# Kernel optimization log

Measured on AMD Instinct MI355X. Metric: run time of the kernel, lower is better.

## Reference

```python
import jax, jax.numpy as jnp
import numpy as np

N_NODES = 100000
N_EDGES = 1600000
D_IN = 128
D_HID = 128
N_CLASS = 10
N_GRAPHS = 512
BN_EPS = 1e-5


def setup_inputs() -> dict:
    key = jax.random.key(0)
    ks = jax.random.split(key, 12)
    x = jax.random.normal(ks[0], (N_NODES, D_IN), dtype=jnp.float32)
    edge_index = jax.random.randint(ks[1], (2, N_EDGES), 0, N_NODES, dtype=jnp.int32)
    idx = jnp.sort(jax.random.randint(ks[2], (N_NODES,), 0, N_GRAPHS, dtype=jnp.int32))
    s = 1.0 / np.sqrt(D_HID)
    W1 = jax.random.uniform(ks[3], (D_IN, D_HID), minval=-s, maxval=s, dtype=jnp.float32)
    b1 = jnp.zeros((D_HID,), jnp.float32)
    W2 = jax.random.uniform(ks[4], (D_HID, D_HID), minval=-s, maxval=s, dtype=jnp.float32)
    b2 = jnp.zeros((D_HID,), jnp.float32)
    W3 = jax.random.uniform(ks[5], (D_HID, D_HID), minval=-s, maxval=s, dtype=jnp.float32)
    b3 = jnp.zeros((D_HID,), jnp.float32)
    W4 = jax.random.uniform(ks[6], (D_HID, N_CLASS), minval=-s, maxval=s, dtype=jnp.float32)
    b4 = jnp.zeros((N_CLASS,), jnp.float32)
    gamma = jnp.ones((D_HID,), jnp.float32)
    beta = jnp.zeros((D_HID,), jnp.float32)
    return {"x": x, "edge_index": edge_index, "idx": idx,
            "W1": W1, "b1": b1, "W2": W2, "b2": b2,
            "W3": W3, "b3": b3, "W4": W4, "b4": b4,
            "gamma": gamma, "beta": beta}


def _agg(h, src, dst):
    # (adj + I) @ h : sum of neighbor features plus self-loop
    return jax.ops.segment_sum(h[src], dst, num_segments=N_NODES) + h


def reference(x, edge_index, idx, W1, b1, W2, b2, W3, b3, W4, b4, gamma, beta):
    src, dst = edge_index[0], edge_index[1]
    z1 = jax.nn.relu(_agg(x, src, dst) @ W1 + b1)          # [N, H] (dropout = identity, eval)
    h = _agg(z1, src, dst) @ W2 + b2                        # [N, H]
    pooled = jax.ops.segment_sum(h, idx, num_segments=N_GRAPHS)  # [G, H] scatter-add readout
    # BatchNorm1d over graph (batch) dimension, training-mode batch stats
    mean = jnp.mean(pooled, axis=0)
    var = jnp.var(pooled, axis=0)
    out = (pooled - mean) * jax.lax.rsqrt(var + BN_EPS) * gamma + beta
    zg = jax.nn.relu(out @ W3 + b3)
    logits = zg @ W4 + b4                                   # [G, C]
    return jax.nn.log_softmax(logits, axis=1)
```

## Files before the change

kernel.cpp:

```cpp
#include <hip/hip_runtime.h>
#include <hip/hip_fp16.h>
#include <math.h>

#define NN 100000
#define NE 1600000
#define DH 128
#define NG 512
#define NC 10
#define NSEG 8
#define SEGN 12500
#define CHE 8192
#define NCH 196
#define MAXDEG 48
#define WPITCH 136

#define NB_HIST (NCH * NSEG)
#define NB_CNT  98
#define NB_GEMM ((NN + 63) / 64)

typedef __attribute__((ext_vector_type(8))) _Float16 f16x8;
typedef __attribute__((ext_vector_type(4))) float f32x4;


__global__ __launch_bounds__(256, 3) void k_build(
    const int* __restrict__ dst, const int* __restrict__ src,
    int* __restrict__ counts, int* __restrict__ csr,
    const int* __restrict__ gidx, int* __restrict__ cnt,
    const float* __restrict__ A, const float* __restrict__ W,
    __half* __restrict__ out) {
    int b = blockIdx.x;
    int t = threadIdx.x;
    if (b < NB_HIST) {
        int seg = b & 7;
        int chunk = b >> 3;
        int lo = seg * SEGN, hi = lo + SEGN;
        int e0 = chunk * CHE;
        int e1 = e0 + CHE < NE ? e0 + CHE : NE;
        for (int e = e0 + t * 4; e < e1; e += 1024) {
            int4 d4 = *(const int4*)(dst + e);
            bool i0 = d4.x >= lo && d4.x < hi;
            bool i1 = d4.y >= lo && d4.y < hi;
            bool i2 = d4.z >= lo && d4.z < hi;
            bool i3 = d4.w >= lo && d4.w < hi;
            int4 s4 = {0, 0, 0, 0};
            if (i0 | i1 | i2 | i3) s4 = *(const int4*)(src + e);
            if (i0) {
                int p = atomicAdd(&counts[d4.x], 1);
                if (p < MAXDEG) csr[d4.x * MAXDEG + p] = s4.x;
            }
            if (i1) {
                int p = atomicAdd(&counts[d4.y], 1);
                if (p < MAXDEG) csr[d4.y * MAXDEG + p] = s4.y;
            }
            if (i2) {
                int p = atomicAdd(&counts[d4.z], 1);
                if (p < MAXDEG) csr[d4.z * MAXDEG + p] = s4.z;
            }
            if (i3) {
                int p = atomicAdd(&counts[d4.w], 1);
                if (p < MAXDEG) csr[d4.w * MAXDEG + p] = s4.w;
            }
        }
    } else if (b < NB_HIST + NB_CNT) {
        int cb = b - NB_HIST;
        int n0 = cb * 1024 + t * 4;
        if (n0 >= NN) return;
        int g = gidx[n0];
        int run = 1;
        for (int j = 1; j < 4; ++j) {
            int n = n0 + j;
            if (n < NN) {
                int gg = gidx[n];
                if (gg == g) {
                    run++;
                } else {
                    atomicAdd(&cnt[g], run);
                    g = gg;
                    run = 1;
                }
            }
        }
        atomicAdd(&cnt[g], run);
    } else {
        __shared__ _Float16 sWT[DH * WPITCH];
        __shared__ __align__(16) _Float16 sOut[4][16][DH];
        int gb = b - (NB_HIST + NB_CNT);
        int wv = t >> 6;
        int lane = t & 63;
        for (int i = t; i < DH * DH; i += 256) {
            int k = i >> 7, n = i & 127;
            sWT[n * WPITCH + k] = (_Float16)W[i];
        }
        __syncthreads();

        int m = lane & 15;
        int quad = lane >> 4;
        int node0 = gb * 64 + wv * 16;
        int nodeA = node0 + m;
        if (nodeA >= NN) nodeA = NN - 1;
        const float* arow = A + (size_t)nodeA * DH;

        f16x8 afrag[4];
#pragma unroll
        for (int kt = 0; kt < 4; ++kt) {
            int k0 = kt * 32 + quad * 8;
            float4 u0 = *(const float4*)(arow + k0);
            float4 u1 = *(const float4*)(arow + k0 + 4);
            afrag[kt][0] = (_Float16)u0.x; afrag[kt][1] = (_Float16)u0.y;
            afrag[kt][2] = (_Float16)u0.z; afrag[kt][3] = (_Float16)u0.w;
            afrag[kt][4] = (_Float16)u1.x; afrag[kt][5] = (_Float16)u1.y;
            afrag[kt][6] = (_Float16)u1.z; afrag[kt][7] = (_Float16)u1.w;
        }

#pragma unroll
        for (int ct = 0; ct < 8; ++ct) {
            f32x4 acc = {0.f, 0.f, 0.f, 0.f};
            int n = ct * 16 + m;
#pragma unroll
            for (int kt = 0; kt < 4; ++kt) {
                int k0 = kt * 32 + quad * 8;
                f16x8 bfrag = *(const f16x8*)&sWT[n * WPITCH + k0];
                acc = __builtin_amdgcn_mfma_f32_16x16x32_f16(afrag[kt], bfrag, acc, 0, 0, 0);
            }
#pragma unroll
            for (int r = 0; r < 4; ++r)
                sOut[wv][quad * 4 + r][ct * 16 + m] = (_Float16)acc[r];
        }
        __syncthreads();

        const uint4* so = (const uint4*)&sOut[wv][0][0];
        for (int i = lane; i < 256; i += 64) {
            int row = i >> 4;
            int node = node0 + row;
            if (node < NN) ((uint4*)out)[(size_t)node * 16 + (i & 15)] = so[i];
        }
    }
}


__device__ __forceinline__ void acc8(float* a, const uint4& v, float m) {
    float2 f;
    f = __half22float2(*(const __half2*)&v.x); a[0] = fmaf(m, f.x, a[0]); a[1] = fmaf(m, f.y, a[1]);
    f = __half22float2(*(const __half2*)&v.y); a[2] = fmaf(m, f.x, a[2]); a[3] = fmaf(m, f.y, a[3]);
    f = __half22float2(*(const __half2*)&v.z); a[4] = fmaf(m, f.x, a[4]); a[5] = fmaf(m, f.y, a[5]);
    f = __half22float2(*(const __half2*)&v.w); a[6] = fmaf(m, f.x, a[6]); a[7] = fmaf(m, f.y, a[7]);
}


__global__ __launch_bounds__(256, 4) void k_agg_h(
    const __half* __restrict__ in, const int* __restrict__ counts,
    const int* __restrict__ csr, const float* __restrict__ bias,
    __half* __restrict__ outA) {
    int t = threadIdx.x;
    int lane = t & 15;
    int node = blockIdx.x * 16 + (t >> 4);
    const uint4* in4 = (const uint4*)in;
    float a[8];
#pragma unroll
    for (int j = 0; j < 8; ++j) a[j] = 0.f;
    uint4 sv = in4[(size_t)node * 16 + lane];
    acc8(a, sv, 1.f);
    int e0 = node * MAXDEG;
    int deg = counts[node];
    deg = deg < MAXDEG ? deg : MAXDEG;
    int e1 = e0 + deg;
    int elast = e1 - 1;
    for (int e = e0; e < e1; e += 8) {
        int idx[8];
        float m[8];
#pragma unroll
        for (int i = 0; i < 8; ++i) {
            int ei = e + i;
            int ec = ei < elast ? ei : elast;
            idx[i] = csr[ec];
            m[i] = (ei < e1) ? 1.f : 0.f;
        }
        uint4 v[8];
#pragma unroll
        for (int i = 0; i < 8; ++i) v[i] = in4[(size_t)idx[i] * 16 + lane];
#pragma unroll
        for (int i = 0; i < 8; ++i) acc8(a, v[i], m[i]);
    }
    float4 b0 = ((const float4*)bias)[lane * 2];
    float4 b1v = ((const float4*)bias)[lane * 2 + 1];
    a[0] = fmaxf(a[0] + b0.x, 0.f);  a[1] = fmaxf(a[1] + b0.y, 0.f);
    a[2] = fmaxf(a[2] + b0.z, 0.f);  a[3] = fmaxf(a[3] + b0.w, 0.f);
    a[4] = fmaxf(a[4] + b1v.x, 0.f); a[5] = fmaxf(a[5] + b1v.y, 0.f);
    a[6] = fmaxf(a[6] + b1v.z, 0.f); a[7] = fmaxf(a[7] + b1v.w, 0.f);
    uint4 o;
    *(__half2*)&o.x = __floats2half2_rn(a[0], a[1]);
    *(__half2*)&o.y = __floats2half2_rn(a[2], a[3]);
    *(__half2*)&o.z = __floats2half2_rn(a[4], a[5]);
    *(__half2*)&o.w = __floats2half2_rn(a[6], a[7]);
    ((uint4*)outA)[(size_t)node * 16 + lane] = o;
}


__global__ __launch_bounds__(256, 4) void k_agg_pool_h(
    const __half* __restrict__ in, const int* __restrict__ counts,
    const int* __restrict__ csr, const int* __restrict__ gidx,
    float* __restrict__ pp8) {
    __shared__ __align__(16) float sA[16][DH];
    int t = threadIdx.x;
    int lane = t & 15;
    int p = t >> 4;
    int node0 = blockIdx.x * 16;
    int node = node0 + p;
    const uint4* in4 = (const uint4*)in;
    float a[8];
#pragma unroll
    for (int j = 0; j < 8; ++j) a[j] = 0.f;
    uint4 sv = in4[(size_t)node * 16 + lane];
    acc8(a, sv, 1.f);
    int e0 = node * MAXDEG;
    int deg = counts[node];
    deg = deg < MAXDEG ? deg : MAXDEG;
    int e1 = e0 + deg;
    int elast = e1 - 1;
    for (int e = e0; e < e1; e += 8) {
        int idx[8];
        float m[8];
#pragma unroll
        for (int i = 0; i < 8; ++i) {
            int ei = e + i;
            int ec = ei < elast ? ei : elast;
            idx[i] = csr[ec];
            m[i] = (ei < e1) ? 1.f : 0.f;
        }
        uint4 v[8];
#pragma unroll
        for (int i = 0; i < 8; ++i) v[i] = in4[(size_t)idx[i] * 16 + lane];
#pragma unroll
        for (int i = 0; i < 8; ++i) acc8(a, v[i], m[i]);
    }
    float4* row = (float4*)&sA[p][lane * 8];
    row[0] = make_float4(a[0], a[1], a[2], a[3]);
    row[1] = make_float4(a[4], a[5], a[6], a[7]);
    __syncthreads();
    if (t < DH) {
        float* pp = pp8 + (size_t)(blockIdx.x & 7) * NG * DH;
        int gprev = gidx[node0];
        float run = 0.f;
        for (int q = 0; q < 16; ++q) {
            int g = gidx[node0 + q];
            if (g != gprev) {
                atomicAdd(&pp[gprev * DH + t], run);
                run = 0.f;
                gprev = g;
            }
            run += sA[q][t];
        }
        atomicAdd(&pp[gprev * DH + t], run);
    }
}


__device__ __forceinline__ void fma4(float4& acc, float s, const float4& wv) {
    acc.x = fmaf(s, wv.x, acc.x);
    acc.y = fmaf(s, wv.y, acc.y);
    acc.z = fmaf(s, wv.z, acc.z);
    acc.w = fmaf(s, wv.w, acc.w);
}


__global__ __launch_bounds__(256, 2) void k_pool_mm(
    const float* __restrict__ pp8, const float* __restrict__ W,
    const float* __restrict__ bias, const int* __restrict__ cnt,
    float* __restrict__ pooled) {
    __shared__ __align__(16) float sW[DH * DH];
    __shared__ __align__(16) float sA[32 * DH];
    int t = threadIdx.x;
    int g0 = blockIdx.x * 32;
    {
        const float4* W4g = (const float4*)W;
        float4* sW4 = (float4*)sW;
        for (int i = t; i < DH * DH / 4; i += 256) sW4[i] = W4g[i];
        const float4* P4 = (const float4*)pp8;
        float4* sA4 = (float4*)sA;
        for (int i = t; i < 32 * DH / 4; i += 256) {
            float4 s;
            s.x = 0.f; s.y = 0.f; s.z = 0.f; s.w = 0.f;
#pragma unroll
            for (int c = 0; c < NSEG; ++c) {
                float4 v = P4[(size_t)c * NG * DH / 4 + (size_t)g0 * DH / 4 + i];
                s.x += v.x; s.y += v.y; s.z += v.z; s.w += v.w;
            }
            sA4[i] = s;
        }
    }
    __syncthreads();

    int c4 = t & 31;
    int n0 = (t >> 5) * 4;
    const float4* sA4 = (const float4*)sA;
    const float4* sW4 = (const float4*)sW;
    float4 acc0, acc1, acc2, acc3;
    acc0.x = acc0.y = acc0.z = acc0.w = 0.f;
    acc1 = acc0; acc2 = acc0; acc3 = acc0;

#pragma unroll 2
    for (int kc = 0; kc < DH / 4; ++kc) {
        float4 a0 = sA4[(n0 + 0) * 32 + kc];
        float4 a1 = sA4[(n0 + 1) * 32 + kc];
        float4 a2 = sA4[(n0 + 2) * 32 + kc];
        float4 a3 = sA4[(n0 + 3) * 32 + kc];
        float4 w0 = sW4[(4 * kc + 0) * 32 + c4];
        float4 w1 = sW4[(4 * kc + 1) * 32 + c4];
        float4 w2 = sW4[(4 * kc + 2) * 32 + c4];
        float4 w3 = sW4[(4 * kc + 3) * 32 + c4];
        fma4(acc0, a0.x, w0); fma4(acc0, a0.y, w1); fma4(acc0, a0.z, w2); fma4(acc0, a0.w, w3);
        fma4(acc1, a1.x, w0); fma4(acc1, a1.y, w1); fma4(acc1, a1.z, w2); fma4(acc1, a1.w, w3);
        fma4(acc2, a2.x, w0); fma4(acc2, a2.y, w1); fma4(acc2, a2.z, w2); fma4(acc2, a2.w, w3);
        fma4(acc3, a3.x, w0); fma4(acc3, a3.y, w1); fma4(acc3, a3.z, w2); fma4(acc3, a3.w, w3);
    }

    float4 b2v = ((const float4*)bias)[c4];
    float c0 = (float)cnt[g0 + n0 + 0];
    float c1 = (float)cnt[g0 + n0 + 1];
    float c2 = (float)cnt[g0 + n0 + 2];
    float c3 = (float)cnt[g0 + n0 + 3];
    fma4(acc0, c0, b2v);
    fma4(acc1, c1, b2v);
    fma4(acc2, c2, b2v);
    fma4(acc3, c3, b2v);

    float4* out4 = (float4*)pooled;
    out4[(size_t)(g0 + n0 + 0) * 32 + c4] = acc0;
    out4[(size_t)(g0 + n0 + 1) * 32 + c4] = acc1;
    out4[(size_t)(g0 + n0 + 2) * 32 + c4] = acc2;
    out4[(size_t)(g0 + n0 + 3) * 32 + c4] = acc3;
}


__global__ void k_bnstats(const float* __restrict__ pooled, float* __restrict__ mean,
                          float* __restrict__ rstd) {
    int c = blockIdx.x;
    int l = threadIdx.x;
    float s = 0.f, s2 = 0.f;
    for (int g = l; g < NG; g += 64) {
        float v = pooled[g * DH + c];
        s += v;
        s2 += v * v;
    }
#pragma unroll
    for (int off = 32; off > 0; off >>= 1) {
        s += __shfl_down(s, off, 64);
        s2 += __shfl_down(s2, off, 64);
    }
    if (l == 0) {
        float m = s * (1.f / NG);
        float var = s2 * (1.f / NG) - m * m;
        mean[c] = m;
        rstd[c] = rsqrtf(var + 1e-5f);
    }
}


__global__ __launch_bounds__(128) void k_tail(
    const float* __restrict__ pooled, const float* __restrict__ mean,
    const float* __restrict__ rstd, const float* __restrict__ gamma,
    const float* __restrict__ beta, const float* __restrict__ W3,
    const float* __restrict__ b3, const float* __restrict__ W4,
    const float* __restrict__ b4, float* __restrict__ out) {
    __shared__ __align__(16) float sW[DH * DH];
    __shared__ float sg[DH];
    __shared__ float sz[DH];
    __shared__ float slog[NC];
    __shared__ float slse;
    int g = blockIdx.x, t = threadIdx.x;
    {
        const float4* W34 = (const float4*)W3;
        float4* sW4 = (float4*)sW;
        for (int i = t; i < DH * DH / 4; i += 128) sW4[i] = W34[i];
    }
    float v = pooled[g * DH + t];
    v = (v - mean[t]) * rstd[t] * gamma[t] + beta[t];
    sg[t] = v;
    __syncthreads();
    float acc = b3[t];
#pragma unroll 4
    for (int k = 0; k < DH; ++k) acc = fmaf(sg[k], sW[k * DH + t], acc);
    sz[t] = fmaxf(acc, 0.f);
    __syncthreads();
    if (t < NC) {
        float a = b4[t];
        for (int k = 0; k < DH; ++k) a = fmaf(sz[k], W4[k * NC + t], a);
        slog[t] = a;
    }
    __syncthreads();
    if (t == 0) {
        float mx = slog[0];
        for (int j = 1; j < NC; ++j) mx = fmaxf(mx, slog[j]);
        float se = 0.f;
        for (int j = 0; j < NC; ++j) se += expf(slog[j] - mx);
        slse = mx + logf(se);
    }
    __syncthreads();
    if (t < NC) out[g * NC + t] = slog[t] - slse;
}


extern "C" void kernel_launch(void* const* d_in, const int* in_sizes, int n_in,
                              void* d_out, int out_size, void* d_ws, size_t ws_size,
                              hipStream_t stream) {
    const float* x = (const float*)d_in[0];
    const int* ei = (const int*)d_in[1];
    const int* src = ei;
    const int* dst = ei + NE;
    const int* gidx = (const int*)d_in[2];
    const float* W1 = (const float*)d_in[3];
    const float* b1 = (const float*)d_in[4];
    const float* W2 = (const float*)d_in[5];
    const float* b2 = (const float*)d_in[6];
    const float* W3 = (const float*)d_in[7];
    const float* b3 = (const float*)d_in[8];
    const float* W4 = (const float*)d_in[9];
    const float* b4 = (const float*)d_in[10];
    const float* gamma = (const float*)d_in[11];
    const float* beta = (const float*)d_in[12];
    float* out = (float*)d_out;

    char* w = (char*)d_ws;
    auto take = [&](size_t bytes) {
        char* p = w;
        w += (bytes + 255) & ~size_t(255);
        return p;
    };
    int* counts = (int*)take((size_t)NN * 4);
    int* cnt = (int*)take((size_t)NG * 4);
    float* pp8 = (float*)take((size_t)NSEG * NG * DH * 4);
    size_t zero_bytes = (size_t)((char*)(pp8 + (size_t)NSEG * NG * DH) - (char*)counts);
    int* csr = (int*)take((size_t)NN * MAXDEG * 4);
    __half* y = (__half*)take((size_t)NN * DH * 2);
    __half* z1 = (__half*)take((size_t)NN * DH * 2);
    float* pooled = (float*)take((size_t)NG * DH * 4);
    float* meanb = (float*)take(DH * 4);
    float* rstdb = (float*)take(DH * 4);

    hipMemsetAsync(counts, 0, zero_bytes, stream);

    k_build<<<NB_HIST + NB_CNT + NB_GEMM, 256, 0, stream>>>(
        dst, src, counts, csr, gidx, cnt, x, W1, y);

    k_agg_h<<<NN / 16, 256, 0, stream>>>(y, counts, csr, b1, z1);

    k_agg_pool_h<<<NN / 16, 256, 0, stream>>>(z1, counts, csr, gidx, pp8);
    k_pool_mm<<<NG / 32, 256, 0, stream>>>(pp8, W2, b2, cnt, pooled);

    k_bnstats<<<DH, 64, 0, stream>>>(pooled, meanb, rstdb);
    k_tail<<<NG, 128, 0, stream>>>(pooled, meanb, rstdb, gamma, beta, W3, b3, W4, b4, out);
}
```

Before: 363.7 us.

## Slice features into 16-column planes and aggregate per node-thread per slice

Feature matrices are stored as eight 16-column slices, each contiguous across nodes. The aggregation kernels switch from 16 lanes per node to one thread per node per slice, so each slice's gather working set (about 3.2 MB) can stay cache-resident. The fused build kernel is split back into separate histogram, count and GEMM launches, and pooling writes to a single partial buffer instead of eight. In exchange each thread issues many small 32-byte gathers, uses more registers, and does serial per-thread loops over edges, which may cost latency hiding and add atomic contention on pooling.

```diff
diff --git a/kernel.cpp b/kernel.cpp
--- a/kernel.cpp
+++ b/kernel.cpp
@@ -9,131 +9,133 @@
 #define NC 10
 #define NSEG 8
 #define SEGN 12500
-#define CHE 8192
-#define NCH 196
+#define CHE 4096
+#define NCH 391
 #define MAXDEG 48
 #define WPITCH 136
-
-#define NB_HIST (NCH * NSEG)
-#define NB_CNT  98
-#define NB_GEMM ((NN + 63) / 64)
+#define NBN 391
 
 typedef __attribute__((ext_vector_type(8))) _Float16 f16x8;
 typedef __attribute__((ext_vector_type(4))) float f32x4;
 
 
-__global__ __launch_bounds__(256, 3) void k_build(
-    const int* __restrict__ dst, const int* __restrict__ src,
-    int* __restrict__ counts, int* __restrict__ csr,
-    const int* __restrict__ gidx, int* __restrict__ cnt,
+__global__ __launch_bounds__(256) void k_hist(const int* __restrict__ dst,
+                                              const int* __restrict__ src,
+                                              int* __restrict__ counts,
+                                              int* __restrict__ csr) {
+    int seg = blockIdx.x & 7;
+    int chunk = blockIdx.x >> 3;
+    int lo = seg * SEGN, hi = lo + SEGN;
+    int e0 = chunk * CHE;
+    int e1 = e0 + CHE < NE ? e0 + CHE : NE;
+    for (int e = e0 + threadIdx.x * 4; e < e1; e += 1024) {
+        int4 d4 = *(const int4*)(dst + e);
+        bool i0 = d4.x >= lo && d4.x < hi;
+        bool i1 = d4.y >= lo && d4.y < hi;
+        bool i2 = d4.z >= lo && d4.z < hi;
+        bool i3 = d4.w >= lo && d4.w < hi;
+        int4 s4 = {0, 0, 0, 0};
+        if (i0 | i1 | i2 | i3) s4 = *(const int4*)(src + e);
+        if (i0) {
+            int p = atomicAdd(&counts[d4.x], 1);
+            if (p < MAXDEG) csr[d4.x * MAXDEG + p] = s4.x;
+        }
+        if (i1) {
+            int p = atomicAdd(&counts[d4.y], 1);
+            if (p < MAXDEG) csr[d4.y * MAXDEG + p] = s4.y;
+        }
+        if (i2) {
+            int p = atomicAdd(&counts[d4.z], 1);
+            if (p < MAXDEG) csr[d4.z * MAXDEG + p] = s4.z;
+        }
+        if (i3) {
+            int p = atomicAdd(&counts[d4.w], 1);
+            if (p < MAXDEG) csr[d4.w * MAXDEG + p] = s4.w;
+        }
+    }
+}
+
+
+__global__ void k_cnt(const int* __restrict__ gidx, int* __restrict__ cnt) {
+    int t = threadIdx.x;
+    int n0 = blockIdx.x * 1024 + t * 4;
+    if (n0 >= NN) return;
+    int g = gidx[n0];
+    int run = 1;
+    for (int j = 1; j < 4; ++j) {
+        int n = n0 + j;
+        if (n < NN) {
+            int gg = gidx[n];
+            if (gg == g) {
+                run++;
+            } else {
+                atomicAdd(&cnt[g], run);
+                g = gg;
+                run = 1;
+            }
+        }
+    }
+    atomicAdd(&cnt[g], run);
+}
+
+
+__global__ __launch_bounds__(256, 3) void k_mm_mfma(
     const float* __restrict__ A, const float* __restrict__ W,
-    __half* __restrict__ out) {
-    int b = blockIdx.x;
+    __half* __restrict__ ys) {
+    __shared__ _Float16 sWT[DH * WPITCH];
+    __shared__ __align__(16) _Float16 sOut[4][16][DH];
     int t = threadIdx.x;
-    if (b < NB_HIST) {
-        int seg = b & 7;
-        int chunk = b >> 3;
-        int lo = seg * SEGN, hi = lo + SEGN;
-        int e0 = chunk * CHE;
-        int e1 = e0 + CHE < NE ? e0 + CHE : NE;
-        for (int e = e0 + t * 4; e < e1; e += 1024) {
-            int4 d4 = *(const int4*)(dst + e);
-            bool i0 = d4.x >= lo && d4.x < hi;
-            bool i1 = d4.y >= lo && d4.y < hi;
-            bool i2 = d4.z >= lo && d4.z < hi;
-            bool i3 = d4.w >= lo && d4.w < hi;
-            int4 s4 = {0, 0, 0, 0};
-            if (i0 | i1 | i2 | i3) s4 = *(const int4*)(src + e);
-            if (i0) {
-                int p = atomicAdd(&counts[d4.x], 1);
-                if (p < MAXDEG) csr[d4.x * MAXDEG + p] = s4.x;
-            }
-            if (i1) {
-                int p = atomicAdd(&counts[d4.y], 1);
-                if (p < MAXDEG) csr[d4.y * MAXDEG + p] = s4.y;
-            }
-            if (i2) {
-                int p = atomicAdd(&counts[d4.z], 1);
-                if (p < MAXDEG) csr[d4.z * MAXDEG + p] = s4.z;
-            }
-            if (i3) {
-                int p = atomicAdd(&counts[d4.w], 1);
-                if (p < MAXDEG) csr[d4.w * MAXDEG + p] = s4.w;
-            }
-        }
-    } else if (b < NB_HIST + NB_CNT) {
-        int cb = b - NB_HIST;
-        int n0 = cb * 1024 + t * 4;
-        if (n0 >= NN) return;
-        int g = gidx[n0];
-        int run = 1;
-        for (int j = 1; j < 4; ++j) {
-            int n = n0 + j;
-            if (n < NN) {
-                int gg = gidx[n];
-                if (gg == g) {
-                    run++;
-                } else {
-                    atomicAdd(&cnt[g], run);
-                    g = gg;
-                    run = 1;
-                }
-            }
-        }
-        atomicAdd(&cnt[g], run);
-    } else {
-        __shared__ _Float16 sWT[DH * WPITCH];
-        __shared__ __align__(16) _Float16 sOut[4][16][DH];
-        int gb = b - (NB_HIST + NB_CNT);
-        int wv = t >> 6;
-        int lane = t & 63;
-        for (int i = t; i < DH * DH; i += 256) {
-            int k = i >> 7, n = i & 127;
-            sWT[n * WPITCH + k] = (_Float16)W[i];
-        }
-        __syncthreads();
-
-        int m = lane & 15;
-        int quad = lane >> 4;
-        int node0 = gb * 64 + wv * 16;
-        int nodeA = node0 + m;
-        if (nodeA >= NN) nodeA = NN - 1;
-        const float* arow = A + (size_t)nodeA * DH;
-
-        f16x8 afrag[4];
+    int wv = t >> 6;
+    int lane = t & 63;
+    for (int i = t; i < DH * DH; i += 256) {
+        int k = i >> 7, n = i & 127;
+        sWT[n * WPITCH + k] = (_Float16)W[i];
+    }
+    __syncthreads();
+
+    int m = lane & 15;
+    int quad = lane >> 4;
+    int node0 = blockIdx.x * 64 + wv * 16;
+    int nodeA = node0 + m;
+    if (nodeA >= NN) nodeA = NN - 1;
+    const float* arow = A + (size_t)nodeA * DH;
+
+    f16x8 afrag[4];
+#pragma unroll
+    for (int kt = 0; kt < 4; ++kt) {
+        int k0 = kt * 32 + quad * 8;
+        float4 u0 = *(const float4*)(arow + k0);
+        float4 u1 = *(const float4*)(arow + k0 + 4);
+        afrag[kt][0] = (_Float16)u0.x; afrag[kt][1] = (_Float16)u0.y;
+        afrag[kt][2] = (_Float16)u0.z; afrag[kt][3] = (_Float16)u0.w;
+        afrag[kt][4] = (_Float16)u1.x; afrag[kt][5] = (_Float16)u1.y;
+        afrag[kt][6] = (_Float16)u1.z; afrag[kt][7] = (_Float16)u1.w;
+    }
+
+#pragma unroll
+    for (int ct = 0; ct < 8; ++ct) {
+        f32x4 acc = {0.f, 0.f, 0.f, 0.f};
+        int n = ct * 16 + m;
 #pragma unroll
         for (int kt = 0; kt < 4; ++kt) {
             int k0 = kt * 32 + quad * 8;
-            float4 u0 = *(const float4*)(arow + k0);
-            float4 u1 = *(const float4*)(arow + k0 + 4);
-            afrag[kt][0] = (_Float16)u0.x; afrag[kt][1] = (_Float16)u0.y;
-            afrag[kt][2] = (_Float16)u0.z; afrag[kt][3] = (_Float16)u0.w;
-            afrag[kt][4] = (_Float16)u1.x; afrag[kt][5] = (_Float16)u1.y;
-            afrag[kt][6] = (_Float16)u1.z; afrag[kt][7] = (_Float16)u1.w;
-        }
-
-#pragma unroll
-        for (int ct = 0; ct < 8; ++ct) {
-            f32x4 acc = {0.f, 0.f, 0.f, 0.f};
-            int n = ct * 16 + m;
-#pragma unroll
-            for (int kt = 0; kt < 4; ++kt) {
-                int k0 = kt * 32 + quad * 8;
-                f16x8 bfrag = *(const f16x8*)&sWT[n * WPITCH + k0];
-                acc = __builtin_amdgcn_mfma_f32_16x16x32_f16(afrag[kt], bfrag, acc, 0, 0, 0);
-            }
-#pragma unroll
-            for (int r = 0; r < 4; ++r)
-                sOut[wv][quad * 4 + r][ct * 16 + m] = (_Float16)acc[r];
-        }
-        __syncthreads();
-
-        const uint4* so = (const uint4*)&sOut[wv][0][0];
-        for (int i = lane; i < 256; i += 64) {
-            int row = i >> 4;
-            int node = node0 + row;
-            if (node < NN) ((uint4*)out)[(size_t)node * 16 + (i & 15)] = so[i];
-        }
+            f16x8 bfrag = *(const f16x8*)&sWT[n * WPITCH + k0];
+            acc = __builtin_amdgcn_mfma_f32_16x16x32_f16(afrag[kt], bfrag, acc, 0, 0, 0);
+        }
+#pragma unroll
+        for (int r = 0; r < 4; ++r)
+            sOut[wv][quad * 4 + r][ct * 16 + m] = (_Float16)acc[r];
+    }
+    __syncthreads();
+
+    const uint4* so = (const uint4*)&sOut[wv][0][0];
+    for (int i = lane; i < 256; i += 64) {
+        int row = i >> 4;
+        int s = (i & 15) >> 1;
+        int h = i & 1;
+        int node = node0 + row;
+        if (node < NN)
+            ((uint4*)ys)[((size_t)s * NN + node) * 2 + h] = so[row * 16 + s * 2 + h];
     }
 }
 
@@ -146,111 +148,130 @@
     f = __half22float2(*(const __half2*)&v.w); a[6] = fmaf(m, f.x, a[6]); a[7] = fmaf(m, f.y, a[7]);
 }
 
-
-__global__ __launch_bounds__(256, 4) void k_agg_h(
-    const __half* __restrict__ in, const int* __restrict__ counts,
+__device__ __forceinline__ void acc16(float* a, const uint4& v0, const uint4& v1, float m) {
+    acc8(a, v0, m);
+    acc8(a + 8, v1, m);
+}
+
+
+__global__ __launch_bounds__(256, 4) void k_agg_s(
+    const __half* __restrict__ ys, const int* __restrict__ counts,
     const int* __restrict__ csr, const float* __restrict__ bias,
-    __half* __restrict__ outA) {
+    __half* __restrict__ z1s) {
+    int s = blockIdx.x & 7;
+    int node = (blockIdx.x >> 3) * 256 + threadIdx.x;
+    bool valid = node < NN;
+    int nodeC = valid ? node : NN - 1;
+    const uint4* base = (const uint4*)ys + (size_t)s * NN * 2;
+    float a[16];
+#pragma unroll
+    for (int j = 0; j < 16; ++j) a[j] = 0.f;
+    acc16(a, base[(size_t)nodeC * 2], base[(size_t)nodeC * 2 + 1], 1.f);
+    int deg = counts[nodeC];
+    deg = deg < MAXDEG ? deg : MAXDEG;
+    int e0 = nodeC * MAXDEG;
+    for (int e = 0; e < deg; e += 4) {
+        int id[4];
+        float m[4];
+#pragma unroll
+        for (int i = 0; i < 4; ++i) {
+            int ei = e + i;
+            int ec = ei < deg - 1 ? ei : deg - 1;
+            id[i] = csr[e0 + ec];
+            m[i] = (ei < deg) ? 1.f : 0.f;
+        }
+        uint4 u[4][2];
+#pragma unroll
+        for (int i = 0; i < 4; ++i) {
+            u[i][0] = base[(size_t)id[i] * 2];
+            u[i][1] = base[(size_t)id[i] * 2 + 1];
+        }
+#pragma unroll
+        for (int i = 0; i < 4; ++i) acc16(a, u[i][0], u[i][1], m[i]);
+    }
+    const float* bs = bias + s * 16;
+#pragma unroll
+    for (int j = 0; j < 16; ++j) a[j] = fmaxf(a[j] + bs[j], 0.f);
+    if (valid) {
+        uint4 o0, o1;
+        *(__half2*)&o0.x = __floats2half2_rn(a[0], a[1]);
+        *(__half2*)&o0.y = __floats2half2_rn(a[2], a[3]);
+        *(__half2*)&o0.z = __floats2half2_rn(a[4], a[5]);
+        *(__half2*)&o0.w = __floats2half2_rn(a[6], a[7]);
+        *(__half2*)&o1.x = __floats2half2_rn(a[8], a[9]);
+        *(__half2*)&o1.y = __floats2half2_rn(a[10], a[11]);
+        *(__half2*)&o1.z = __floats2half2_rn(a[12], a[13]);
+        *(__half2*)&o1.w = __floats2half2_rn(a[14], a[15]);
+        uint4* zb = (uint4*)z1s + (size_t)s * NN * 2;
+        zb[(size_t)node * 2] = o0;
+        zb[(size_t)node * 2 + 1] = o1;
+    }
+}
+
+
+__global__ __launch_bounds__(256, 4) void k_agg_pool_s(
+    const __half* __restrict__ z1s, const int* __restrict__ counts,
+    const int* __restrict__ csr, const int* __restrict__ gidx,
+    float* __restrict__ pp) {
+    __shared__ float sP[256][16];
+    int s = blockIdx.x & 7;
     int t = threadIdx.x;
-    int lane = t & 15;
-    int node = blockIdx.x * 16 + (t >> 4);
-    const uint4* in4 = (const uint4*)in;
-    float a[8];
-#pragma unroll
-    for (int j = 0; j < 8; ++j) a[j] = 0.f;
-    uint4 sv = in4[(size_t)node * 16 + lane];
-    acc8(a, sv, 1.f);
-    int e0 = node * MAXDEG;
-    int deg = counts[node];
+    int node0 = (blockIdx.x >> 3) * 256;
+    int node = node0 + t;
+    bool valid = node < NN;
+    int nodeC = valid ? node : NN - 1;
+    const uint4* base = (const uint4*)z1s + (size_t)s * NN * 2;
+    float a[16];
+#pragma unroll
+    for (int j = 0; j < 16; ++j) a[j] = 0.f;
+    acc16(a, base[(size_t)nodeC * 2], base[(size_t)nodeC * 2 + 1], 1.f);
+    int deg = counts[nodeC];
     deg = deg < MAXDEG ? deg : MAXDEG;
-    int e1 = e0 + deg;
-    int elast = e1 - 1;
-    for (int e = e0; e < e1; e += 8) {
-        int idx[8];
-        float m[8];
-#pragma unroll
-        for (int i = 0; i < 8; ++i) {
+    int e0 = nodeC * MAXDEG;
+    for (int e = 0; e < deg; e += 4) {
+        int id[4];
+        float m[4];
+#pragma unroll
+        for (int i = 0; i < 4; ++i) {
             int ei = e + i;
-            int ec = ei < elast ? ei : elast;
-            idx[i] = csr[ec];
-            m[i] = (ei < e1) ? 1.f : 0.f;
-        }
-        uint4 v[8];
-#pragma unroll
-        for (int i = 0; i < 8; ++i) v[i] = in4[(size_t)idx[i] * 16 + lane];
-#pragma unroll
-        for (int i = 0; i < 8; ++i) acc8(a, v[i], m[i]);
-    }
-    float4 b0 = ((const float4*)bias)[lane * 2];
-    float4 b1v = ((const float4*)bias)[lane * 2 + 1];
-    a[0] = fmaxf(a[0] + b0.x, 0.f);  a[1] = fmaxf(a[1] + b0.y, 0.f);
-    a[2] = fmaxf(a[2] + b0.z, 0.f);  a[3] = fmaxf(a[3] + b0.w, 0.f);
-    a[4] = fmaxf(a[4] + b1v.x, 0.f); a[5] = fmaxf(a[5] + b1v.y, 0.f);
-    a[6] = fmaxf(a[6] + b1v.z, 0.f); a[7] = fmaxf(a[7] + b1v.w, 0.f);
-    uint4 o;
-    *(__half2*)&o.x = __floats2half2_rn(a[0], a[1]);
-    *(__half2*)&o.y = __floats2half2_rn(a[2], a[3]);
-    *(__half2*)&o.z = __floats2half2_rn(a[4], a[5]);
-    *(__half2*)&o.w = __floats2half2_rn(a[6], a[7]);
-    ((uint4*)outA)[(size_t)node * 16 + lane] = o;
-}
-
-
-__global__ __launch_bounds__(256, 4) void k_agg_pool_h(
-    const __half* __restrict__ in, const int* __restrict__ counts,
-    const int* __restrict__ csr, const int* __restrict__ gidx,
-    float* __restrict__ pp8) {
-    __shared__ __align__(16) float sA[16][DH];
-    int t = threadIdx.x;
-    int lane = t & 15;
-    int p = t >> 4;
-    int node0 = blockIdx.x * 16;
-    int node = node0 + p;
-    const uint4* in4 = (const uint4*)in;
-    float a[8];
-#pragma unroll
-    for (int j = 0; j < 8; ++j) a[j] = 0.f;
-    uint4 sv = in4[(size_t)node * 16 + lane];
-    acc8(a, sv, 1.f);
-    int e0 = node * MAXDEG;
-    int deg = counts[node];
-    deg = deg < MAXDEG ? deg : MAXDEG;
-    int e1 = e0 + deg;
-    int elast = e1 - 1;
-    for (int e = e0; e < e1; e += 8) {
-        int idx[8];
-        float m[8];
-#pragma unroll
-        for (int i = 0; i < 8; ++i) {
-            int ei = e + i;
-            int ec = ei < elast ? ei : elast;
-            idx[i] = csr[ec];
-            m[i] = (ei < e1) ? 1.f : 0.f;
-        }
-        uint4 v[8];
-#pragma unroll
-        for (int i = 0; i < 8; ++i) v[i] = in4[(size_t)idx[i] * 16 + lane];
-#pragma unroll
-        for (int i = 0; i < 8; ++i) acc8(a, v[i], m[i]);
-    }
-    float4* row = (float4*)&sA[p][lane * 8];
-    row[0] = make_float4(a[0], a[1], a[2], a[3]);
-    row[1] = make_float4(a[4], a[5], a[6], a[7]);
-    __syncthreads();
-    if (t < DH) {
-        float* pp = pp8 + (size_t)(blockIdx.x & 7) * NG * DH;
-        int gprev = gidx[node0];
+            int ec = ei < deg - 1 ? ei : deg - 1;
+            id[i] = csr[e0 + ec];
+            m[i] = (ei < deg) ? 1.f : 0.f;
+        }
+        uint4 u[4][2];
+#pragma unroll
+        for (int i = 0; i < 4; ++i) {
+            u[i][0] = base[(size_t)id[i] * 2];
+            u[i][1] = base[(size_t)id[i] * 2 + 1];
+        }
+#pragma unroll
+        for (int i = 0; i < 4; ++i) acc16(a, u[i][0], u[i][1], m[i]);
+    }
+    if (!valid) {
+#pragma unroll
+        for (int j = 0; j < 16; ++j) a[j] = 0.f;
+    }
+#pragma unroll
+    for (int j = 0; j < 16; ++j) sP[t][j] = a[j];
+    __syncthreads();
+    int chunk = t >> 4;
+    int c = t & 15;
+    int nb = node0 + chunk * 16;
+    if (nb < NN) {
+        int gprev = gidx[nb];
         float run = 0.f;
-        for (int q = 0; q < 16; ++q) {
-            int g = gidx[node0 + q];
+        for (int i = 0; i < 16; ++i) {
+            int n = nb + i;
+            if (n >= NN) break;
+            int g = gidx[n];
             if (g != gprev) {
-                atomicAdd(&pp[gprev * DH + t], run);
+                atomicAdd(&pp[gprev * DH + s * 16 + c], run);
                 run = 0.f;
                 gprev = g;
             }
-            run += sA[q][t];
-        }
-        atomicAdd(&pp[gprev * DH + t], run);
+            run += sP[chunk * 16 + i][c];
+        }
+        atomicAdd(&pp[gprev * DH + s * 16 + c], run);
     }
 }
 
@@ -264,7 +285,7 @@
 
 
 __global__ __launch_bounds__(256, 2) void k_pool_mm(
-    const float* __restrict__ pp8, const float* __restrict__ W,
+    const float* __restrict__ pp, const float* __restrict__ W,
     const float* __restrict__ bias, const int* __restrict__ cnt,
     float* __restrict__ pooled) {
     __shared__ __align__(16) float sW[DH * DH];
@@ -275,18 +296,9 @@
         const float4* W4g = (const float4*)W;
         float4* sW4 = (float4*)sW;
         for (int i = t; i < DH * DH / 4; i += 256) sW4[i] = W4g[i];
-        const float4* P4 = (const float4*)pp8;
+        const float4* P4 = (const float4*)pp;
         float4* sA4 = (float4*)sA;
-        for (int i = t; i < 32 * DH / 4; i += 256) {
-            float4 s;
-            s.x = 0.f; s.y = 0.f; s.z = 0.f; s.w = 0.f;
-#pragma unroll
-            for (int c = 0; c < NSEG; ++c) {
-                float4 v = P4[(size_t)c * NG * DH / 4 + (size_t)g0 * DH / 4 + i];
-                s.x += v.x; s.y += v.y; s.z += v.z; s.w += v.w;
-            }
-            sA4[i] = s;
-        }
+        for (int i = t; i < 32 * DH / 4; i += 256) sA4[i] = P4[(size_t)g0 * DH / 4 + i];
     }
     __syncthreads();
 
@@ -428,24 +440,25 @@
     };
     int* counts = (int*)take((size_t)NN * 4);
     int* cnt = (int*)take((size_t)NG * 4);
-    float* pp8 = (float*)take((size_t)NSEG * NG * DH * 4);
-    size_t zero_bytes = (size_t)((char*)(pp8 + (size_t)NSEG * NG * DH) - (char*)counts);
+    float* pp = (float*)take((size_t)NG * DH * 4);
+    size_t zero_bytes = (size_t)((char*)(pp + (size_t)NG * DH) - (char*)counts);
     int* csr = (int*)take((size_t)NN * MAXDEG * 4);
-    __half* y = (__half*)take((size_t)NN * DH * 2);
-    __half* z1 = (__half*)take((size_t)NN * DH * 2);
+    __half* ys = (__half*)take((size_t)NN * DH * 2);
+    __half* z1s = (__half*)take((size_t)NN * DH * 2);
     float* pooled = (float*)take((size_t)NG * DH * 4);
     float* meanb = (float*)take(DH * 4);
     float* rstdb = (float*)take(DH * 4);
 
     hipMemsetAsync(counts, 0, zero_bytes, stream);
 
-    k_build<<<NB_HIST + NB_CNT + NB_GEMM, 256, 0, stream>>>(
-        dst, src, counts, csr, gidx, cnt, x, W1, y);
-
-    k_agg_h<<<NN / 16, 256, 0, stream>>>(y, counts, csr, b1, z1);
-
-    k_agg_pool_h<<<NN / 16, 256, 0, stream>>>(z1, counts, csr, gidx, pp8);
-    k_pool_mm<<<NG / 32, 256, 0, stream>>>(pp8, W2, b2, cnt, pooled);
+    k_hist<<<NCH * NSEG, 256, 0, stream>>>(dst, src, counts, csr);
+    k_cnt<<<98, 256, 0, stream>>>(gidx, cnt);
+
+    k_mm_mfma<<<(NN + 63) / 64, 256, 0, stream>>>(x, W1, ys);
+    k_agg_s<<<NBN * NSEG, 256, 0, stream>>>(ys, counts, csr, b1, z1s);
+
+    k_agg_pool_s<<<NBN * NSEG, 256, 0, stream>>>(z1s, counts, csr, gidx, pp);
+    k_pool_mm<<<NG / 32, 256, 0, stream>>>(pp, W2, b2, cnt, pooled);
 
     k_bnstats<<<DH, 64, 0, stream>>>(pooled, meanb, rstdb);
     k_tail<<<NG, 128, 0, stream>>>(pooled, meanb, rstdb, gamma, beta, W3, b3, W4, b4, out);
```

Measured after the change: 554.5 us. 52.4% more time.
